# Optimization experiments

Measured on AMD Instinct MI355X. Metric: run time of the kernel, lower is better.

The kernel has to match this reference:

```python
import jax, jax.numpy as jnp
import numpy as np

D_MODEL = 1024
H = 16
D_HEAD = D_MODEL // H


def setup_inputs() -> dict:
    key = jax.random.key(0)
    ks = jax.random.split(key, 9)
    B, S = 2, 2048
    x = jax.random.normal(ks[0], (B, S, D_MODEL), dtype=jnp.float32)
    s = 1.0 / np.sqrt(D_HEAD)
    # per-head Q/K/V linears, stacked: W[h, out, in], b[h, out] (torch Linear: y = x W^T + b)
    Wq = jax.random.normal(ks[1], (H, D_HEAD, D_HEAD), dtype=jnp.float32) * s
    bq = jax.random.normal(ks[2], (H, D_HEAD), dtype=jnp.float32) * 0.01
    Wk = jax.random.normal(ks[3], (H, D_HEAD, D_HEAD), dtype=jnp.float32) * s
    bk = jax.random.normal(ks[4], (H, D_HEAD), dtype=jnp.float32) * 0.01
    Wv = jax.random.normal(ks[5], (H, D_HEAD, D_HEAD), dtype=jnp.float32) * s
    bv = jax.random.normal(ks[6], (H, D_HEAD), dtype=jnp.float32) * 0.01
    Wo = jax.random.normal(ks[7], (D_MODEL, D_MODEL), dtype=jnp.float32) / np.sqrt(D_MODEL)
    bo = jax.random.normal(ks[8], (D_MODEL,), dtype=jnp.float32) * 0.01
    return {"x": x, "Wq": Wq, "bq": bq, "Wk": Wk, "bk": bk,
            "Wv": Wv, "bv": bv, "Wo": Wo, "bo": bo}


def reference(x, Wq, bq, Wk, bk, Wv, bv, Wo, bo):
    B, S, D = x.shape
    xh = x.reshape(B, S, H, D_HEAD)  # split along feature dim, head-major
    q = jnp.einsum('bshi,hoi->bsho', xh, Wq) + bq
    k = jnp.einsum('bshi,hoi->bsho', xh, Wk) + bk
    v = jnp.einsum('bshi,hoi->bsho', xh, Wv) + bv
    scale = 1.0 / jnp.sqrt(jnp.asarray(D_HEAD, dtype=x.dtype))  # source scales by sqrt(d_model//h)
    scores = jnp.einsum('bqhd,bkhd->bhqk', q, k) * scale
    causal = jnp.tril(jnp.ones((S, S), dtype=bool))
    scores = jnp.where(causal, scores, -jnp.inf)
    attn = jax.nn.softmax(scores, axis=-1)
    out = jnp.einsum('bhqk,bkhd->bqhd', attn, v).reshape(B, S, D)
    return out @ Wo.T + bo
```

## Files before the change

### kernel.cpp

```cpp
#include <hip/hip_runtime.h>
#include <cstddef>

#define Bc 2
#define Sc 2048
#define Dc 1024
#define Hc 16
#define QSC 0.18033688011112042f

typedef short short8 __attribute__((ext_vector_type(8)));
typedef float floatx4 __attribute__((ext_vector_type(4)));
typedef unsigned short ushort_t;

#if __has_builtin(__builtin_amdgcn_exp2f)
#define EXP2F(x) __builtin_amdgcn_exp2f(x)
#else
#define EXP2F(x) exp2f(x)
#endif

__device__ __forceinline__ unsigned pack2bf(float a, float b) {
    unsigned ua = __float_as_uint(a) + 0x8000u;
    unsigned ub = __float_as_uint(b) + 0x8000u;
    return __builtin_amdgcn_perm(ub, ua, 0x07060302u);
}
__device__ __forceinline__ ushort_t f2bf(float f) {
    return (ushort_t)((__float_as_uint(f) + 0x8000u) >> 16);
}
__device__ __forceinline__ unsigned cvtpk2bf(float a, float b) {
    unsigned r;
    asm("v_cvt_pk_bf16_f32 %0, %1, %2" : "=v"(r) : "v"(a), "v"(b));
    return r;
}

__global__ __launch_bounds__(256) void qkv_kernel(
    const float* __restrict__ x,
    const float* __restrict__ Wq, const float* __restrict__ Wk, const float* __restrict__ Wv,
    const float* __restrict__ bq, const float* __restrict__ bk, const float* __restrict__ bv,
    ushort_t* __restrict__ Qb, ushort_t* __restrict__ Kf, ushort_t* __restrict__ Vf)
{
    const int blk = blockIdx.x;
    const int st = blk & 31, h = (blk >> 5) & 15, b = blk >> 9;
    const int bh = b * Hc + h, s0 = st * 64;
    const int tid = threadIdx.x, wid = tid >> 6, lane = tid & 63;
    const int lr = lane & 15, quad = lane >> 4;

    __shared__ ushort_t Xs[64 * 72];
    __shared__ ushort_t Wsh[3 * 64 * 72];

    {
        int row = tid >> 2, cg = tid & 3;
        const float* xp = x + ((size_t)(b * Sc + s0 + row)) * Dc + h * 64 + cg * 16;
        float4 v0 = *(const float4*)xp;
        float4 v1 = *(const float4*)(xp + 4);
        float4 v2 = *(const float4*)(xp + 8);
        float4 v3 = *(const float4*)(xp + 12);
        uint4 p0, p1;
        p0.x = pack2bf(v0.x, v0.y); p0.y = pack2bf(v0.z, v0.w);
        p0.z = pack2bf(v1.x, v1.y); p0.w = pack2bf(v1.z, v1.w);
        p1.x = pack2bf(v2.x, v2.y); p1.y = pack2bf(v2.z, v2.w);
        p1.z = pack2bf(v3.x, v3.y); p1.w = pack2bf(v3.z, v3.w);
        *(uint4*)(Xs + row * 72 + cg * 16) = p0;
        *(uint4*)(Xs + row * 72 + cg * 16 + 8) = p1;
    }
    {
#pragma unroll
        for (int s = 0; s < 6; ++s) {
            int c = tid + s * 256;
            int w = c >> 9, rem = c & 511, row = rem >> 3, part = rem & 7;
            const float* wp = (w == 0 ? Wq : (w == 1 ? Wk : Wv))
                              + (size_t)h * 4096 + row * 64 + part * 8;
            float4 v0 = *(const float4*)wp;
            float4 v1 = *(const float4*)(wp + 4);
            uint4 o;
            o.x = pack2bf(v0.x, v0.y); o.y = pack2bf(v0.z, v0.w);
            o.z = pack2bf(v1.x, v1.y); o.w = pack2bf(v1.z, v1.w);
            *(uint4*)(Wsh + (w * 64 + row) * 72 + part * 8) = o;
        }
    }
    __syncthreads();

    short8 af0 = *(const short8*)(Xs + (wid * 16 + lr) * 72 + quad * 8);
    short8 af1 = *(const short8*)(Xs + (wid * 16 + lr) * 72 + 32 + quad * 8);

    const float* bias3[3] = {bq + h * 64, bk + h * 64, bv + h * 64};
    const int row = tid >> 2, cg = tid & 3;

#pragma unroll
    for (int w = 0; w < 3; ++w) {
        ushort_t* Ot = Wsh + w * 64 * 72;
        short8 bf0[4], bf1[4];
#pragma unroll
        for (int n = 0; n < 4; ++n) {
            const ushort_t* wrow = Ot + (n * 16 + lr) * 72;
            bf0[n] = *(const short8*)(wrow + quad * 8);
            bf1[n] = *(const short8*)(wrow + 32 + quad * 8);
        }
        floatx4 acc[4];
#pragma unroll
        for (int n = 0; n < 4; ++n) {
            floatx4 z = {0.f, 0.f, 0.f, 0.f};
            acc[n] = __builtin_amdgcn_mfma_f32_16x16x32_bf16(af0, bf0[n], z, 0, 0, 0);
            acc[n] = __builtin_amdgcn_mfma_f32_16x16x32_bf16(af1, bf1[n], acc[n], 0, 0, 0);
        }
        __syncthreads();
        if (w < 2) {
#pragma unroll
            for (int n = 0; n < 4; ++n) {
                float bias = bias3[w][n * 16 + lr];
#pragma unroll
                for (int r = 0; r < 4; ++r) {
                    float val = acc[n][r] + bias;
                    if (w == 0) val *= QSC;
                    Ot[(wid * 16 + quad * 4 + r) * 72 + n * 16 + lr] = f2bf(val);
                }
            }
        } else {
#pragma unroll
            for (int n = 0; n < 4; ++n) {
                float bias = bias3[2][n * 16 + lr];
                uint2 pw;
                pw.x = pack2bf(acc[n][0] + bias, acc[n][1] + bias);
                pw.y = pack2bf(acc[n][2] + bias, acc[n][3] + bias);
                *(uint2*)(Ot + (n * 16 + lr) * 72 + wid * 16 + quad * 4) = pw;
            }
        }
        __syncthreads();
        if (w == 0) {
            const ushort_t* srcp = Ot + row * 72 + cg * 16;
            uint4 d0 = *(const uint4*)srcp;
            uint4 d1 = *(const uint4*)(srcp + 8);
            ushort_t* dst = Qb + ((size_t)bh * Sc + s0 + row) * 64 + cg * 16;
            *(uint4*)dst = d0;
            *(uint4*)(dst + 8) = d1;
        } else if (w == 1) {
            uint4 d0 = *(const uint4*)(Ot + (4 * lr + wid) * 72 + 8 * quad);
            uint4 d1 = *(const uint4*)(Ot + (4 * lr + wid) * 72 + 32 + 8 * quad);
            ushort_t* dstb = Kf + ((size_t)(bh * 32 + st)) * 4096 + wid * 1024 + lane * 8;
            *(uint4*)dstb = d0;
            *(uint4*)(dstb + 512) = d1;
        } else {
            uint4 d0 = *(const uint4*)(Ot + (wid * 16 + lr) * 72 + 16 * quad);
            uint4 d1 = *(const uint4*)(Ot + (wid * 16 + lr) * 72 + 16 * quad + 8);
            ushort_t* dstb = Vf + ((size_t)(bh * 32 + st)) * 4096 + wid * 1024 + lane * 8;
            *(uint4*)dstb = d0;
            *(uint4*)(dstb + 512) = d1;
        }
    }
}

#define LOADK(dst, t) do {                                                    \
    const ushort_t* Kt_ = Kfb + (size_t)(t) * 4096;                           \
    dst[0][0] = *(const short8*)(Kt_);                                        \
    dst[0][1] = *(const short8*)(Kt_ + 512);                                  \
    dst[1][0] = *(const short8*)(Kt_ + 1024);                                 \
    dst[1][1] = *(const short8*)(Kt_ + 1536);                                 \
    dst[2][0] = *(const short8*)(Kt_ + 2048);                                 \
    dst[2][1] = *(const short8*)(Kt_ + 2560);                                 \
    dst[3][0] = *(const short8*)(Kt_ + 3072);                                 \
    dst[3][1] = *(const short8*)(Kt_ + 3584);                                 \
} while (0)

#define ATTN_STEP(kc, kn, kt) do {                                            \
    const bool hasB = ((kt) <= qtb);                                          \
    const ushort_t* Vt = Vfb + (size_t)(kt) * 4096;                           \
    short8 vf[4][2];                                                          \
    _Pragma("unroll")                                                         \
    for (int n = 0; n < 4; ++n) {                                             \
        vf[n][0] = *(const short8*)(Vt + n * 1024);                           \
        vf[n][1] = *(const short8*)(Vt + n * 1024 + 512);                     \
    }                                                                         \
    floatx4 sA[4], sB[4];                                                     \
    __builtin_amdgcn_s_setprio(1);                                            \
    _Pragma("unroll")                                                         \
    for (int kg = 0; kg < 4; ++kg) {                                          \
        floatx4 z = {0.f, 0.f, 0.f, 0.f};                                     \
        floatx4 t0 = __builtin_amdgcn_mfma_f32_16x16x32_bf16(kc[kg][0], qfa0, z, 0, 0, 0); \
        sA[kg] = __builtin_amdgcn_mfma_f32_16x16x32_bf16(kc[kg][1], qfa1, t0, 0, 0, 0);    \
    }                                                                         \
    if (hasB) {                                                               \
        _Pragma("unroll")                                                     \
        for (int kg = 0; kg < 4; ++kg) {                                      \
            floatx4 z = {0.f, 0.f, 0.f, 0.f};                                 \
            floatx4 t0 = __builtin_amdgcn_mfma_f32_16x16x32_bf16(kc[kg][0], qfb0, z, 0, 0, 0); \
            sB[kg] = __builtin_amdgcn_mfma_f32_16x16x32_bf16(kc[kg][1], qfb1, t0, 0, 0, 0);    \
        }                                                                     \
    }                                                                         \
    __builtin_amdgcn_s_setprio(0);                                            \
            \
    LOADK(kn, (kt) < qta ? (kt) + 1 : qta);                                   \
    const int qrow = wid * 16 + lr;                                           \
    if ((kt) == qta) {                                                        \
        _Pragma("unroll")                                                     \
        for (int kg = 0; kg < 4; ++kg)                                        \
            _Pragma("unroll")                                                 \
            for (int r = 0; r < 4; ++r)                                       \
                if (16 * quad + 4 * r + kg > qrow) sA[kg][r] = -1e30f;        \
    }                                                                         \
    if (hasB && (kt) == qtb) {                                                \
        _Pragma("unroll")                                                     \
        for (int kg = 0; kg < 4; ++kg)                                        \
            _Pragma("unroll")                                                 \
            for (int r = 0; r < 4; ++r)                                       \
                if (16 * quad + 4 * r + kg > qrow) sB[kg][r] = -1e30f;        \
    }                                                                         \
    {                                                                         \
        float e[4][4];                                                        \
        _Pragma("unroll")                                                     \
        for (int kg = 0; kg < 4; ++kg)                                        \
            _Pragma("unroll")                                                 \
            for (int r = 0; r < 4; ++r) e[kg][r] = EXP2F(sA[kg][r]);          \
        union { uint4 u; short8 s; } p0, p1;                                  \
        p0.u.x = cvtpk2bf(e[0][0], e[1][0]); p0.u.y = cvtpk2bf(e[2][0], e[3][0]); \
        p0.u.z = cvtpk2bf(e[0][1], e[1][1]); p0.u.w = cvtpk2bf(e[2][1], e[3][1]); \
        p1.u.x = cvtpk2bf(e[0][2], e[1][2]); p1.u.y = cvtpk2bf(e[2][2], e[3][2]); \
        p1.u.z = cvtpk2bf(e[0][3], e[1][3]); p1.u.w = cvtpk2bf(e[2][3], e[3][3]); \
        __builtin_amdgcn_s_setprio(1);                                        \
        _Pragma("unroll")                                                     \
        for (int n = 0; n < 4; ++n) {                                         \
            oA[n] = __builtin_amdgcn_mfma_f32_16x16x32_bf16(p0.s, vf[n][0], oA[n], 0, 0, 0); \
            oA[n] = __builtin_amdgcn_mfma_f32_16x16x32_bf16(p1.s, vf[n][1], oA[n], 0, 0, 0); \
        }                                                                     \
        laccA = __builtin_amdgcn_mfma_f32_16x16x32_bf16(p0.s, ones1, laccA, 0, 0, 0); \
        laccA = __builtin_amdgcn_mfma_f32_16x16x32_bf16(p1.s, ones1, laccA, 0, 0, 0); \
        __builtin_amdgcn_s_setprio(0);                                        \
    }                                                                         \
    if (hasB) {                                                               \
        float e[4][4];                                                        \
        _Pragma("unroll")                                                     \
        for (int kg = 0; kg < 4; ++kg)                                        \
            _Pragma("unroll")                                                 \
            for (int r = 0; r < 4; ++r) e[kg][r] = EXP2F(sB[kg][r]);          \
        union { uint4 u; short8 s; } p0, p1;                                  \
        p0.u.x = cvtpk2bf(e[0][0], e[1][0]); p0.u.y = cvtpk2bf(e[2][0], e[3][0]); \
        p0.u.z = cvtpk2bf(e[0][1], e[1][1]); p0.u.w = cvtpk2bf(e[2][1], e[3][1]); \
        p1.u.x = cvtpk2bf(e[0][2], e[1][2]); p1.u.y = cvtpk2bf(e[2][2], e[3][2]); \
        p1.u.z = cvtpk2bf(e[0][3], e[1][3]); p1.u.w = cvtpk2bf(e[2][3], e[3][3]); \
        __builtin_amdgcn_s_setprio(1);                                        \
        _Pragma("unroll")                                                     \
        for (int n = 0; n < 4; ++n) {                                         \
            oB[n] = __builtin_amdgcn_mfma_f32_16x16x32_bf16(p0.s, vf[n][0], oB[n], 0, 0, 0); \
            oB[n] = __builtin_amdgcn_mfma_f32_16x16x32_bf16(p1.s, vf[n][1], oB[n], 0, 0, 0); \
        }                                                                     \
        laccB = __builtin_amdgcn_mfma_f32_16x16x32_bf16(p0.s, ones1, laccB, 0, 0, 0); \
        laccB = __builtin_amdgcn_mfma_f32_16x16x32_bf16(p1.s, ones1, laccB, 0, 0, 0); \
        __builtin_amdgcn_s_setprio(0);                                        \
    }                                                                         \
} while (0)

__global__ __launch_bounds__(256, 2) void attn_kernel(
    const ushort_t* __restrict__ Qg, const ushort_t* __restrict__ Kfg,
    const ushort_t* __restrict__ Vfg, ushort_t* __restrict__ Actx)
{
    const int blk = blockIdx.x;
    const int x = blk & 7;
    const int bh = ((blk >> 3) & 3) * 8 + x;
    const int fbase = (blk >> 5) & 7;
    const int f = (blk < 256) ? fbase : 15 - fbase;
    const int b = bh >> 4, h = bh & 15;
    const int qta = 31 - f, qtb = f;
    const int s0a = qta * 64, s0b = qtb * 64;
    const int tid = threadIdx.x, wid = tid >> 6, lane = tid & 63;
    const int lr = lane & 15, quad = lane >> 4;

    const ushort_t* Kfb = Kfg + (size_t)bh * 32 * 4096 + lane * 8;
    const ushort_t* Vfb = Vfg + (size_t)bh * 32 * 4096 + lane * 8;

    const ushort_t* QrA = Qg + ((size_t)bh * Sc + s0a + wid * 16 + lr) * 64;
    const ushort_t* QrB = Qg + ((size_t)bh * Sc + s0b + wid * 16 + lr) * 64;
    short8 qfa0 = *(const short8*)(QrA + quad * 8);
    short8 qfa1 = *(const short8*)(QrA + 32 + quad * 8);
    short8 qfb0 = *(const short8*)(QrB + quad * 8);
    short8 qfb1 = *(const short8*)(QrB + 32 + quad * 8);

    floatx4 oA[4], oB[4];
    floatx4 laccA = {0.f, 0.f, 0.f, 0.f}, laccB = {0.f, 0.f, 0.f, 0.f};
    const short ONE_BF = (short)0x3F80;
    const short8 ones1 = {ONE_BF, ONE_BF, ONE_BF, ONE_BF, ONE_BF, ONE_BF, ONE_BF, ONE_BF};
#pragma unroll
    for (int n = 0; n < 4; ++n) { oA[n] = floatx4{0,0,0,0}; oB[n] = floatx4{0,0,0,0}; }

    short8 kbuf0[4][2], kbuf1[4][2];
    LOADK(kbuf0, 0);

    int kt = 0;
    for (;;) {
        ATTN_STEP(kbuf0, kbuf1, kt);
        if (++kt > qta) break;
        ATTN_STEP(kbuf1, kbuf0, kt);
        if (++kt > qta) break;
    }

#pragma unroll
    for (int r = 0; r < 4; ++r) {
        float iA = 1.f / laccA[r];
        float iB = 1.f / laccB[r];
        int rowA = s0a + wid * 16 + quad * 4 + r;
        int rowB = s0b + wid * 16 + quad * 4 + r;
        ushort_t* dA = Actx + ((size_t)(b * Sc + rowA)) * Dc + h * 64 + lr;
        ushort_t* dB = Actx + ((size_t)(b * Sc + rowB)) * Dc + h * 64 + lr;
#pragma unroll
        for (int n = 0; n < 4; ++n) {
            dA[n * 16] = f2bf(oA[n][r] * iA);
            dB[n * 16] = f2bf(oB[n][r] * iB);
        }
    }
}

__global__ __launch_bounds__(256, 2) void proj_kernel(
    const ushort_t* __restrict__ Ab, const float* __restrict__ WoF,
    const float* __restrict__ bo, float* __restrict__ out)
{
    const int bn = blockIdx.x & 15, bm = blockIdx.x >> 4;
    const int tid = threadIdx.x, wid = tid >> 6, lane = tid & 63;
    const int lr = lane & 15, quad = lane >> 4;
    const int wm = wid * 32;

    __shared__ ushort_t As[128 * 72];
    __shared__ ushort_t Bs[64 * 72];

    floatx4 acc[2][4];
#pragma unroll
    for (int i = 0; i < 2; ++i)
#pragma unroll
        for (int n = 0; n < 4; ++n) acc[i][n] = floatx4{0.f, 0.f, 0.f, 0.f};

    const ushort_t* Ag = Ab + (size_t)bm * 128 * 1024;
    const float* Wg = WoF + (size_t)bn * 64 * 1024;

    const int arow = tid >> 1, acol = (tid & 1) * 32;
    const int brow = tid >> 2, bcol = (tid & 3) * 16;

    short8 a0, a1, a2, a3;
    float4 b0, b1, b2, b3;

    {
        const ushort_t* ap = Ag + (size_t)arow * 1024 + acol;
        a0 = *(const short8*)(ap);      a1 = *(const short8*)(ap + 8);
        a2 = *(const short8*)(ap + 16); a3 = *(const short8*)(ap + 24);
        const float* bp = Wg + (size_t)brow * 1024 + bcol;
        b0 = *(const float4*)(bp);      b1 = *(const float4*)(bp + 4);
        b2 = *(const float4*)(bp + 8);  b3 = *(const float4*)(bp + 12);
        ushort_t* aw = As + arow * 72 + acol;
        *(short8*)(aw) = a0;      *(short8*)(aw + 8) = a1;
        *(short8*)(aw + 16) = a2; *(short8*)(aw + 24) = a3;
        uint4 w0, w1;
        w0.x = pack2bf(b0.x, b0.y); w0.y = pack2bf(b0.z, b0.w);
        w0.z = pack2bf(b1.x, b1.y); w0.w = pack2bf(b1.z, b1.w);
        w1.x = pack2bf(b2.x, b2.y); w1.y = pack2bf(b2.z, b2.w);
        w1.z = pack2bf(b3.x, b3.y); w1.w = pack2bf(b3.z, b3.w);
        ushort_t* bw = Bs + brow * 72 + bcol;
        *(uint4*)(bw) = w0;
        *(uint4*)(bw + 8) = w1;
    }
    __syncthreads();

    for (int k0 = 0; k0 < 1024; k0 += 64) {
        short8 fa0[2], fa1[2], fb[2][4];
#pragma unroll
        for (int kh = 0; kh < 2; ++kh) {
            fa0[kh] = *(const short8*)(As + (wm + lr) * 72 + kh * 32 + quad * 8);
            fa1[kh] = *(const short8*)(As + (wm + 16 + lr) * 72 + kh * 32 + quad * 8);
#pragma unroll
            for (int n = 0; n < 4; ++n)
                fb[kh][n] = *(const short8*)(Bs + (n * 16 + lr) * 72 + kh * 32 + quad * 8);
        }

        if (k0 < 960) {
            int k1 = k0 + 64;
            const ushort_t* ap = Ag + (size_t)arow * 1024 + k1 + acol;
            a0 = *(const short8*)(ap);      a1 = *(const short8*)(ap + 8);
            a2 = *(const short8*)(ap + 16); a3 = *(const short8*)(ap + 24);
            const float* bp = Wg + (size_t)brow * 1024 + k1 + bcol;
            b0 = *(const float4*)(bp);      b1 = *(const float4*)(bp + 4);
            b2 = *(const float4*)(bp + 8);  b3 = *(const float4*)(bp + 12);
        }

#pragma unroll
        for (int kh = 0; kh < 2; ++kh)
#pragma unroll
            for (int n = 0; n < 4; ++n) {
                acc[0][n] = __builtin_amdgcn_mfma_f32_16x16x32_bf16(fa0[kh], fb[kh][n], acc[0][n], 0, 0, 0);
                acc[1][n] = __builtin_amdgcn_mfma_f32_16x16x32_bf16(fa1[kh], fb[kh][n], acc[1][n], 0, 0, 0);
            }
        __syncthreads();
        if (k0 < 960) {
            ushort_t* aw = As + arow * 72 + acol;
            *(short8*)(aw) = a0;      *(short8*)(aw + 8) = a1;
            *(short8*)(aw + 16) = a2; *(short8*)(aw + 24) = a3;
            uint4 w0, w1;
            w0.x = pack2bf(b0.x, b0.y); w0.y = pack2bf(b0.z, b0.w);
            w0.z = pack2bf(b1.x, b1.y); w0.w = pack2bf(b1.z, b1.w);
            w1.x = pack2bf(b2.x, b2.y); w1.y = pack2bf(b2.z, b2.w);
            w1.z = pack2bf(b3.x, b3.y); w1.w = pack2bf(b3.z, b3.w);
            ushort_t* bw = Bs + brow * 72 + bcol;
            *(uint4*)(bw) = w0;
            *(uint4*)(bw + 8) = w1;
            __syncthreads();
        }
    }

#pragma unroll
    for (int i = 0; i < 2; ++i) {
        int mrow = bm * 128 + wm + i * 16 + quad * 4;
#pragma unroll
        for (int n = 0; n < 4; ++n) {
            int col = bn * 64 + n * 16 + lr;
            float bias = bo[col];
#pragma unroll
            for (int r = 0; r < 4; ++r)
                out[(size_t)(mrow + r) * 1024 + col] = acc[i][n][r] + bias;
        }
    }
}

extern "C" void kernel_launch(void* const* d_in, const int* in_sizes, int n_in,
                              void* d_out, int out_size, void* d_ws, size_t ws_size,
                              hipStream_t stream)
{
    (void)in_sizes; (void)n_in; (void)out_size; (void)ws_size;
    const float* x  = (const float*)d_in[0];
    const float* Wq = (const float*)d_in[1];
    const float* bq = (const float*)d_in[2];
    const float* Wk = (const float*)d_in[3];
    const float* bk = (const float*)d_in[4];
    const float* Wv = (const float*)d_in[5];
    const float* bv = (const float*)d_in[6];
    const float* Wo = (const float*)d_in[7];
    const float* bo = (const float*)d_in[8];
    float* out = (float*)d_out;

    const size_t N4 = (size_t)Bc * Hc * Sc * 64;
    ushort_t* base  = (ushort_t*)d_ws;
    ushort_t* Qb    = base;
    ushort_t* Kf    = base + N4;
    ushort_t* Vf    = base + 2 * N4;
    ushort_t* Actx  = base + 3 * N4;

    qkv_kernel<<<dim3(Bc * Hc * (Sc / 64)), dim3(256), 0, stream>>>(
        x, Wq, Wk, Wv, bq, bk, bv, Qb, Kf, Vf);
    attn_kernel<<<dim3(512), dim3(256), 0, stream>>>(Qb, Kf, Vf, Actx);
    proj_kernel<<<dim3(32 * 16), dim3(256), 0, stream>>>(Actx, Wo, bo, out);
}
```

Baseline: 138.0 us.

## Split paired causal q-tiles into separate blocks with one tile per block

The attention kernel previously had each block process two query tiles (a long one and its short complement) to balance the causal workload. Now each block handles a single 64-row query tile, the grid doubles to 1024 blocks, and launch bounds rise to three blocks per SIMD group. This cuts register pressure and the dual-path branching, so occupancy can rise. The cost is losing the built-in load balance and sharing of K/V loads between the two tiles. Blocks are ordered longest tile first to soften the tail imbalance.

Result: slower. 150.4 us (+9.0%).

```diff
diff --git a/kernel.cpp b/kernel.cpp
--- a/kernel.cpp
+++ b/kernel.cpp
@@ -160,7 +160,6 @@
 } while (0)
 
 #define ATTN_STEP(kc, kn, kt) do {                                            \
-    const bool hasB = ((kt) <= qtb);                                          \
     const ushort_t* Vt = Vfb + (size_t)(kt) * 4096;                           \
     short8 vf[4][2];                                                          \
     _Pragma("unroll")                                                         \
@@ -168,7 +167,7 @@
         vf[n][0] = *(const short8*)(Vt + n * 1024);                           \
         vf[n][1] = *(const short8*)(Vt + n * 1024 + 512);                     \
     }                                                                         \
-    floatx4 sA[4], sB[4];                                                     \
+    floatx4 sA[4];                                                            \
     __builtin_amdgcn_s_setprio(1);                                            \
     _Pragma("unroll")                                                         \
     for (int kg = 0; kg < 4; ++kg) {                                          \
@@ -176,31 +175,16 @@
         floatx4 t0 = __builtin_amdgcn_mfma_f32_16x16x32_bf16(kc[kg][0], qfa0, z, 0, 0, 0); \
         sA[kg] = __builtin_amdgcn_mfma_f32_16x16x32_bf16(kc[kg][1], qfa1, t0, 0, 0, 0);    \
     }                                                                         \
-    if (hasB) {                                                               \
-        _Pragma("unroll")                                                     \
-        for (int kg = 0; kg < 4; ++kg) {                                      \
-            floatx4 z = {0.f, 0.f, 0.f, 0.f};                                 \
-            floatx4 t0 = __builtin_amdgcn_mfma_f32_16x16x32_bf16(kc[kg][0], qfb0, z, 0, 0, 0); \
-            sB[kg] = __builtin_amdgcn_mfma_f32_16x16x32_bf16(kc[kg][1], qfb1, t0, 0, 0, 0);    \
-        }                                                                     \
-    }                                                                         \
     __builtin_amdgcn_s_setprio(0);                                            \
             \
     LOADK(kn, (kt) < qta ? (kt) + 1 : qta);                                   \
-    const int qrow = wid * 16 + lr;                                           \
     if ((kt) == qta) {                                                        \
+        const int qrow = wid * 16 + lr;                                       \
         _Pragma("unroll")                                                     \
         for (int kg = 0; kg < 4; ++kg)                                        \
             _Pragma("unroll")                                                 \
             for (int r = 0; r < 4; ++r)                                       \
                 if (16 * quad + 4 * r + kg > qrow) sA[kg][r] = -1e30f;        \
-    }                                                                         \
-    if (hasB && (kt) == qtb) {                                                \
-        _Pragma("unroll")                                                     \
-        for (int kg = 0; kg < 4; ++kg)                                        \
-            _Pragma("unroll")                                                 \
-            for (int r = 0; r < 4; ++r)                                       \
-                if (16 * quad + 4 * r + kg > qrow) sB[kg][r] = -1e30f;        \
     }                                                                         \
     {                                                                         \
         float e[4][4];                                                        \
@@ -223,41 +207,18 @@
         laccA = __builtin_amdgcn_mfma_f32_16x16x32_bf16(p1.s, ones1, laccA, 0, 0, 0); \
         __builtin_amdgcn_s_setprio(0);                                        \
     }                                                                         \
-    if (hasB) {                                                               \
-        float e[4][4];                                                        \
-        _Pragma("unroll")                                                     \
-        for (int kg = 0; kg < 4; ++kg)                                        \
-            _Pragma("unroll")                                                 \
-            for (int r = 0; r < 4; ++r) e[kg][r] = EXP2F(sB[kg][r]);          \
-        union { uint4 u; short8 s; } p0, p1;                                  \
-        p0.u.x = cvtpk2bf(e[0][0], e[1][0]); p0.u.y = cvtpk2bf(e[2][0], e[3][0]); \
-        p0.u.z = cvtpk2bf(e[0][1], e[1][1]); p0.u.w = cvtpk2bf(e[2][1], e[3][1]); \
-        p1.u.x = cvtpk2bf(e[0][2], e[1][2]); p1.u.y = cvtpk2bf(e[2][2], e[3][2]); \
-        p1.u.z = cvtpk2bf(e[0][3], e[1][3]); p1.u.w = cvtpk2bf(e[2][3], e[3][3]); \
-        __builtin_amdgcn_s_setprio(1);                                        \
-        _Pragma("unroll")                                                     \
-        for (int n = 0; n < 4; ++n) {                                         \
-            oB[n] = __builtin_amdgcn_mfma_f32_16x16x32_bf16(p0.s, vf[n][0], oB[n], 0, 0, 0); \
-            oB[n] = __builtin_amdgcn_mfma_f32_16x16x32_bf16(p1.s, vf[n][1], oB[n], 0, 0, 0); \
-        }                                                                     \
-        laccB = __builtin_amdgcn_mfma_f32_16x16x32_bf16(p0.s, ones1, laccB, 0, 0, 0); \
-        laccB = __builtin_amdgcn_mfma_f32_16x16x32_bf16(p1.s, ones1, laccB, 0, 0, 0); \
-        __builtin_amdgcn_s_setprio(0);                                        \
-    }                                                                         \
 } while (0)
 
-__global__ __launch_bounds__(256, 2) void attn_kernel(
+__global__ __launch_bounds__(256, 3) void attn_kernel(
     const ushort_t* __restrict__ Qg, const ushort_t* __restrict__ Kfg,
     const ushort_t* __restrict__ Vfg, ushort_t* __restrict__ Actx)
 {
     const int blk = blockIdx.x;
     const int x = blk & 7;
     const int bh = ((blk >> 3) & 3) * 8 + x;
-    const int fbase = (blk >> 5) & 7;
-    const int f = (blk < 256) ? fbase : 15 - fbase;
+    const int qta = 31 - (blk >> 5);
     const int b = bh >> 4, h = bh & 15;
-    const int qta = 31 - f, qtb = f;
-    const int s0a = qta * 64, s0b = qtb * 64;
+    const int s0a = qta * 64;
     const int tid = threadIdx.x, wid = tid >> 6, lane = tid & 63;
     const int lr = lane & 15, quad = lane >> 4;
 
@@ -265,18 +226,15 @@
     const ushort_t* Vfb = Vfg + (size_t)bh * 32 * 4096 + lane * 8;
 
     const ushort_t* QrA = Qg + ((size_t)bh * Sc + s0a + wid * 16 + lr) * 64;
-    const ushort_t* QrB = Qg + ((size_t)bh * Sc + s0b + wid * 16 + lr) * 64;
     short8 qfa0 = *(const short8*)(QrA + quad * 8);
     short8 qfa1 = *(const short8*)(QrA + 32 + quad * 8);
-    short8 qfb0 = *(const short8*)(QrB + quad * 8);
-    short8 qfb1 = *(const short8*)(QrB + 32 + quad * 8);
-
-    floatx4 oA[4], oB[4];
-    floatx4 laccA = {0.f, 0.f, 0.f, 0.f}, laccB = {0.f, 0.f, 0.f, 0.f};
+
+    floatx4 oA[4];
+    floatx4 laccA = {0.f, 0.f, 0.f, 0.f};
     const short ONE_BF = (short)0x3F80;
     const short8 ones1 = {ONE_BF, ONE_BF, ONE_BF, ONE_BF, ONE_BF, ONE_BF, ONE_BF, ONE_BF};
 #pragma unroll
-    for (int n = 0; n < 4; ++n) { oA[n] = floatx4{0,0,0,0}; oB[n] = floatx4{0,0,0,0}; }
+    for (int n = 0; n < 4; ++n) oA[n] = floatx4{0, 0, 0, 0};
 
     short8 kbuf0[4][2], kbuf1[4][2];
     LOADK(kbuf0, 0);
@@ -292,16 +250,11 @@
 #pragma unroll
     for (int r = 0; r < 4; ++r) {
         float iA = 1.f / laccA[r];
-        float iB = 1.f / laccB[r];
         int rowA = s0a + wid * 16 + quad * 4 + r;
-        int rowB = s0b + wid * 16 + quad * 4 + r;
         ushort_t* dA = Actx + ((size_t)(b * Sc + rowA)) * Dc + h * 64 + lr;
-        ushort_t* dB = Actx + ((size_t)(b * Sc + rowB)) * Dc + h * 64 + lr;
-#pragma unroll
-        for (int n = 0; n < 4; ++n) {
+#pragma unroll
+        for (int n = 0; n < 4; ++n)
             dA[n * 16] = f2bf(oA[n][r] * iA);
-            dB[n * 16] = f2bf(oB[n][r] * iB);
-        }
     }
 }
 
@@ -437,6 +390,6 @@
 
     qkv_kernel<<<dim3(Bc * Hc * (Sc / 64)), dim3(256), 0, stream>>>(
         x, Wq, Wk, Wv, bq, bk, bv, Qb, Kf, Vf);
-    attn_kernel<<<dim3(512), dim3(256), 0, stream>>>(Qb, Kf, Vf, Actx);
+    attn_kernel<<<dim3(1024), dim3(256), 0, stream>>>(Qb, Kf, Vf, Actx);
     proj_kernel<<<dim3(32 * 16), dim3(256), 0, stream>>>(Actx, Wo, bo, out);
 }
```
